# Optimization experiments

Hardware: AMD Instinct MI355X
Metric: run time of the kernel (lower is better)

Reference implementation:

```python
import jax, jax.numpy as jnp
import numpy as np

N_NODES = 50000
N_EDGES = 800000


def gat_layer(x, src, dst, W, al, ar, b, activation):
    # x: [N, F_in], W: [F_in, H*D], al/ar: [H, D], b: [H*D]
    H, D = al.shape
    n = x.shape[0]
    h = (x @ W).reshape(n, H, D)                      # [N, H, D]
    el = jnp.sum(h * al, axis=-1)                     # [N, H]
    er = jnp.sum(h * ar, axis=-1)                     # [N, H]
    e = jax.nn.leaky_relu(el[src] + er[dst], 0.2)     # [E, H]
    # segment softmax over incoming edges of each dst node
    m = jax.ops.segment_max(e, dst, num_segments=n)   # [N, H]
    ex = jnp.exp(e - m[dst])                          # [E, H]
    s = jax.ops.segment_sum(ex, dst, num_segments=n)  # [N, H]
    a = ex / s[dst]                                   # [E, H]
    msg = h[src] * a[:, :, None]                      # [E, H, D]
    out = jax.ops.segment_sum(msg, dst, num_segments=n) + b.reshape(1, H, D)
    return activation(out) if activation is not None else out


def setup_inputs() -> dict:
    key = jax.random.key(0)
    ks = jax.random.split(key, 12)
    feat = jax.random.normal(ks[0], (N_NODES, 128), dtype=jnp.float32)
    src = jax.random.randint(ks[1], (N_EDGES,), 0, N_NODES)
    dst = jax.random.randint(ks[2], (N_EDGES,), 0, N_NODES)
    sc = 0.1
    return {
        "feat": feat, "src": src, "dst": dst,
        "W1": jax.random.normal(ks[3], (128, 256), jnp.float32) * sc,
        "al1": jax.random.normal(ks[4], (4, 64), jnp.float32) * sc,
        "ar1": jax.random.normal(ks[5], (4, 64), jnp.float32) * sc,
        "b1": jnp.zeros((256,), jnp.float32),
        "W2": jax.random.normal(ks[6], (256, 256), jnp.float32) * sc,
        "al2": jax.random.normal(ks[7], (4, 64), jnp.float32) * sc,
        "ar2": jax.random.normal(ks[8], (4, 64), jnp.float32) * sc,
        "b2": jnp.zeros((256,), jnp.float32),
        "W3": jax.random.normal(ks[9], (256, 8), jnp.float32) * sc,
        "al3": jax.random.normal(ks[10], (1, 8), jnp.float32) * sc,
        "ar3": jax.random.normal(ks[11], (1, 8), jnp.float32) * sc,
        "b3": jnp.zeros((8,), jnp.float32),
    }


def reference(feat, src, dst, W1, al1, ar1, b1, W2, al2, ar2, b2, W3, al3, ar3, b3):
    n = feat.shape[0]
    elu = jax.nn.elu
    h = gat_layer(feat, src, dst, W1, al1, ar1, b1, elu).reshape(n, -1)  # flatten heads
    h = gat_layer(h, src, dst, W2, al2, ar2, b2, elu).reshape(n, -1)
    h = gat_layer(h, src, dst, W3, al3, ar3, b3, None)                   # [N, 1, out]
    return h.mean(axis=1)                                               # head mean -> [N, out]
```

## Files before the change

### kernel.cpp

```cpp
#include <hip/hip_runtime.h>
#include <math.h>


typedef _Float16 half8 __attribute__((ext_vector_type(8)));
typedef _Float16 half4 __attribute__((ext_vector_type(4)));
typedef float    floatx4 __attribute__((ext_vector_type(4)));

#define SLOT_CAP 48

__device__ __forceinline__ float leaky02(float x) { return x > 0.f ? x : 0.2f * x; }

__global__ void build_prep(const int* __restrict__ src, const int* __restrict__ dst,
                           int* __restrict__ cnt, unsigned short* __restrict__ slots,
                           const float* __restrict__ W1, _Float16* __restrict__ W1T,
                           const float* __restrict__ W2, _Float16* __restrict__ W2T,
                           int E, int GE) {
    int b = blockIdx.x;
    if (b < GE) {
        int i = b * 256 + threadIdx.x;
        if (i < E) {
            int d = dst[i];
            int p = atomicAdd(&cnt[d], 1);
            if (p < SLOT_CAP) slots[d * SLOT_CAP + p] = (unsigned short)src[i];
        }
    } else {
        int i = (b - GE) * 256 + threadIdx.x;
        if (i < 128 * 256) {
            int m = i >> 7, k = i & 127;
            W1T[i] = (_Float16)W1[k * 256 + m];
        } else {
            int j = i - 128 * 256;
            if (j < 256 * 256) {
                int m = j >> 8, k = j & 255;
                W2T[j] = (_Float16)W2[k * 256 + m];
            }
        }
    }
}

#define GBM 128
#define GBK 32

template <bool AF32>
__global__ __launch_bounds__(256)
void gemm_mfma(const void* __restrict__ Ap, const _Float16* __restrict__ BT,
               _Float16* __restrict__ C, int N, int K) {
    __shared__ _Float16 As[GBM][GBK + 8];
    __shared__ _Float16 Bs[GBM][GBK + 8];
    int tid  = threadIdx.x;
    int wave = tid >> 6, lane = tid & 63;
    int quad = lane >> 4, l16 = lane & 15;
    int row0 = blockIdx.y * GBM;
    int col0 = blockIdx.x * GBM;

    floatx4 acc[8][2];
    #pragma unroll
    for (int i = 0; i < 8; ++i)
        #pragma unroll
        for (int j = 0; j < 2; ++j)
            #pragma unroll
            for (int e = 0; e < 4; ++e) acc[i][j][e] = 0.f;

    for (int k0 = 0; k0 < K; k0 += GBK) {
        if (AF32) {
            const float* Af = (const float*)Ap;
            #pragma unroll
            for (int it = 0; it < 4; ++it) {
                int s = it * 256 + tid;
                int r = s >> 3, off = (s & 7) * 4;
                float4 v = make_float4(0.f, 0.f, 0.f, 0.f);
                int gr = row0 + r;
                if (gr < N) v = *(const float4*)&Af[(size_t)gr * K + k0 + off];
                half4 hv;
                hv[0] = (_Float16)v.x; hv[1] = (_Float16)v.y;
                hv[2] = (_Float16)v.z; hv[3] = (_Float16)v.w;
                *(half4*)&As[r][off] = hv;
            }
        } else {
            const _Float16* Ah = (const _Float16*)Ap;
            #pragma unroll
            for (int it = 0; it < 2; ++it) {
                int s = it * 256 + tid;
                int r = s >> 2, off = (s & 3) * 8;
                half8 v;
                #pragma unroll
                for (int q = 0; q < 8; ++q) v[q] = (_Float16)0.f;
                int gr = row0 + r;
                if (gr < N) v = *(const half8*)&Ah[(size_t)gr * K + k0 + off];
                *(half8*)&As[r][off] = v;
            }
        }
        #pragma unroll
        for (int it = 0; it < 2; ++it) {
            int s = it * 256 + tid;
            int r = s >> 2, off = (s & 3) * 8;
            half8 w = *(const half8*)&BT[(size_t)(col0 + r) * K + k0 + off];
            *(half8*)&Bs[r][off] = w;
        }
        __syncthreads();
        half8 bfrag[2];
        #pragma unroll
        for (int ct = 0; ct < 2; ++ct)
            bfrag[ct] = *(const half8*)&Bs[wave * 32 + ct * 16 + l16][quad * 8];
        #pragma unroll
        for (int rt = 0; rt < 8; ++rt) {
            half8 afrag = *(const half8*)&As[rt * 16 + l16][quad * 8];
            acc[rt][0] = __builtin_amdgcn_mfma_f32_16x16x32_f16(afrag, bfrag[0], acc[rt][0], 0, 0, 0);
            acc[rt][1] = __builtin_amdgcn_mfma_f32_16x16x32_f16(afrag, bfrag[1], acc[rt][1], 0, 0, 0);
        }
        __syncthreads();
    }
    #pragma unroll
    for (int rt = 0; rt < 8; ++rt) {
        #pragma unroll
        for (int reg = 0; reg < 4; ++reg) {
            int gr = row0 + rt * 16 + quad * 4 + reg;
            if (gr < N) {
                #pragma unroll
                for (int ct = 0; ct < 2; ++ct) {
                    int gc = col0 + wave * 32 + ct * 16 + l16;
                    C[(size_t)gr * 256 + gc] = (_Float16)acc[rt][ct][reg];
                }
            }
        }
    }
}

__global__ __launch_bounds__(256)
void attn_lr(const _Float16* __restrict__ h16, const float* __restrict__ al,
             const float* __restrict__ ar, float* __restrict__ el,
             float* __restrict__ er, int NH) {
    int wid = (blockIdx.x * 256 + threadIdx.x) >> 6;
    int lane = threadIdx.x & 63;
    int r = lane >> 3, c = lane & 7;
    int row = wid * 8 + r;
    if (row >= NH) return;
    int hd = row & 3;
    half8 hv = *(const half8*)&h16[(size_t)row * 64 + c * 8];
    const float* alp = &al[hd * 64 + c * 8];
    const float* arp = &ar[hd * 64 + c * 8];
    float l = 0.f, rr = 0.f;
    #pragma unroll
    for (int q = 0; q < 8; ++q) {
        float v = (float)hv[q];
        l  += v * alp[q];
        rr += v * arp[q];
    }
    l  += __shfl_xor(l, 1);  l  += __shfl_xor(l, 2);  l  += __shfl_xor(l, 4);
    rr += __shfl_xor(rr, 1); rr += __shfl_xor(rr, 2); rr += __shfl_xor(rr, 4);
    if (c == 0) { el[row] = l; er[row] = rr; }
}

__global__ __launch_bounds__(256)
void gat_agg(const _Float16* __restrict__ h16, const float* __restrict__ el,
             const float* __restrict__ er, const int* __restrict__ cnt,
             const unsigned short* __restrict__ slots, const float* __restrict__ bias,
             _Float16* __restrict__ out, int N) {
    __shared__ int   sbuf[8][32];
    __shared__ float wbuf[8][32][4];
    int tid = threadIdx.x;
    int l32 = tid & 31;
    int g = tid >> 5;
    int node = blockIdx.x * 8 + g;
    if (node >= N) return;
    int deg = min(cnt[node], SLOT_CAP);
    int beg = node * SLOT_CAP, end = beg + deg;
    int hd = l32 >> 3;

    float4 ern4 = *(const float4*)&er[node * 4];
    float er0 = ern4.x, er1 = ern4.y, er2 = ern4.z, er3 = ern4.w;

    const _Float16* hb = h16 + l32 * 8;
    float acc[8] = {};

    if (deg <= 32) {
        bool act = l32 < deg;
        int sv = 0;
        float e0 = -INFINITY, e1 = -INFINITY, e2 = -INFINITY, e3 = -INFINITY;
        if (act) {
            sv = slots[beg + l32];
            float4 elv = *(const float4*)&el[sv * 4];
            e0 = leaky02(elv.x + er0);
            e1 = leaky02(elv.y + er1);
            e2 = leaky02(elv.z + er2);
            e3 = leaky02(elv.w + er3);
        }
        float m0 = e0, m1 = e1, m2 = e2, m3 = e3;
        #pragma unroll
        for (int msk = 1; msk < 32; msk <<= 1) {
            m0 = fmaxf(m0, __shfl_xor(m0, msk));
            m1 = fmaxf(m1, __shfl_xor(m1, msk));
            m2 = fmaxf(m2, __shfl_xor(m2, msk));
            m3 = fmaxf(m3, __shfl_xor(m3, msk));
        }
        float x0 = act ? __expf(e0 - m0) : 0.f;
        float x1 = act ? __expf(e1 - m1) : 0.f;
        float x2 = act ? __expf(e2 - m2) : 0.f;
        float x3 = act ? __expf(e3 - m3) : 0.f;
        float s0 = x0, s1 = x1, s2 = x2, s3 = x3;
        #pragma unroll
        for (int msk = 1; msk < 32; msk <<= 1) {
            s0 += __shfl_xor(s0, msk);
            s1 += __shfl_xor(s1, msk);
            s2 += __shfl_xor(s2, msk);
            s3 += __shfl_xor(s3, msk);
        }
        float i0 = s0 > 0.f ? 1.f / s0 : 0.f;
        float i1 = s1 > 0.f ? 1.f / s1 : 0.f;
        float i2 = s2 > 0.f ? 1.f / s2 : 0.f;
        float i3 = s3 > 0.f ? 1.f / s3 : 0.f;
        if (act) {
            sbuf[g][l32] = sv;
            wbuf[g][l32][0] = x0 * i0;
            wbuf[g][l32][1] = x1 * i1;
            wbuf[g][l32][2] = x2 * i2;
            wbuf[g][l32][3] = x3 * i3;
        }
        int t = 0;
        for (; t + 4 <= deg; t += 4) {
            int sa = sbuf[g][t],     sb = sbuf[g][t + 1];
            int sc = sbuf[g][t + 2], sd = sbuf[g][t + 3];
            float wa = wbuf[g][t][hd],     wb = wbuf[g][t + 1][hd];
            float wc = wbuf[g][t + 2][hd], wd = wbuf[g][t + 3][hd];
            half8 va = *(const half8*)&hb[(size_t)sa * 256];
            half8 vb = *(const half8*)&hb[(size_t)sb * 256];
            half8 vc = *(const half8*)&hb[(size_t)sc * 256];
            half8 vd = *(const half8*)&hb[(size_t)sd * 256];
            #pragma unroll
            for (int q = 0; q < 8; ++q)
                acc[q] += wa * (float)va[q] + wb * (float)vb[q]
                        + wc * (float)vc[q] + wd * (float)vd[q];
        }
        for (; t < deg; ++t) {
            int s = sbuf[g][t];
            float w = wbuf[g][t][hd];
            half8 v = *(const half8*)&hb[(size_t)s * 256];
            #pragma unroll
            for (int q = 0; q < 8; ++q) acc[q] += w * (float)v[q];
        }
    } else {
        float m0 = -INFINITY, m1 = -INFINITY, m2 = -INFINITY, m3 = -INFINITY;
        for (int j = beg + l32; j < end; j += 32) {
            int sv = slots[j];
            float4 elv = *(const float4*)&el[sv * 4];
            m0 = fmaxf(m0, leaky02(elv.x + er0));
            m1 = fmaxf(m1, leaky02(elv.y + er1));
            m2 = fmaxf(m2, leaky02(elv.z + er2));
            m3 = fmaxf(m3, leaky02(elv.w + er3));
        }
        #pragma unroll
        for (int msk = 1; msk < 32; msk <<= 1) {
            m0 = fmaxf(m0, __shfl_xor(m0, msk));
            m1 = fmaxf(m1, __shfl_xor(m1, msk));
            m2 = fmaxf(m2, __shfl_xor(m2, msk));
            m3 = fmaxf(m3, __shfl_xor(m3, msk));
        }
        float s0 = 0.f, s1 = 0.f, s2 = 0.f, s3 = 0.f;
        for (int j = beg + l32; j < end; j += 32) {
            int sv = slots[j];
            float4 elv = *(const float4*)&el[sv * 4];
            s0 += __expf(leaky02(elv.x + er0) - m0);
            s1 += __expf(leaky02(elv.y + er1) - m1);
            s2 += __expf(leaky02(elv.z + er2) - m2);
            s3 += __expf(leaky02(elv.w + er3) - m3);
        }
        #pragma unroll
        for (int msk = 1; msk < 32; msk <<= 1) {
            s0 += __shfl_xor(s0, msk);
            s1 += __shfl_xor(s1, msk);
            s2 += __shfl_xor(s2, msk);
            s3 += __shfl_xor(s3, msk);
        }
        float mh  = (hd & 2) ? ((hd & 1) ? m3 : m2) : ((hd & 1) ? m1 : m0);
        float sh_ = (hd & 2) ? ((hd & 1) ? s3 : s2) : ((hd & 1) ? s1 : s0);
        float erh = (hd & 2) ? ((hd & 1) ? er3 : er2) : ((hd & 1) ? er1 : er0);
        float ih  = sh_ > 0.f ? 1.f / sh_ : 0.f;
        int j = beg;
        for (; j + 4 <= end; j += 4) {
            int sa = slots[j], sb = slots[j + 1], sc = slots[j + 2], sd = slots[j + 3];
            float wa = __expf(leaky02(el[sa * 4 + hd] + erh) - mh) * ih;
            float wb = __expf(leaky02(el[sb * 4 + hd] + erh) - mh) * ih;
            float wc = __expf(leaky02(el[sc * 4 + hd] + erh) - mh) * ih;
            float wd = __expf(leaky02(el[sd * 4 + hd] + erh) - mh) * ih;
            half8 va = *(const half8*)&hb[(size_t)sa * 256];
            half8 vb = *(const half8*)&hb[(size_t)sb * 256];
            half8 vc = *(const half8*)&hb[(size_t)sc * 256];
            half8 vd = *(const half8*)&hb[(size_t)sd * 256];
            #pragma unroll
            for (int q = 0; q < 8; ++q)
                acc[q] += wa * (float)va[q] + wb * (float)vb[q]
                        + wc * (float)vc[q] + wd * (float)vd[q];
        }
        for (; j < end; ++j) {
            int sv = slots[j];
            float w = __expf(leaky02(el[sv * 4 + hd] + erh) - mh) * ih;
            half8 v = *(const half8*)&hb[(size_t)sv * 256];
            #pragma unroll
            for (int q = 0; q < 8; ++q) acc[q] += w * (float)v[q];
        }
    }

    half8 o;
    #pragma unroll
    for (int q = 0; q < 8; ++q) {
        float v = acc[q] + bias[l32 * 8 + q];
        v = v > 0.f ? v : (__expf(v) - 1.f);
        o[q] = (_Float16)v;
    }
    *(half8*)&out[(size_t)node * 256 + l32 * 8] = o;
}

__global__ __launch_bounds__(256)
void gemm3_attn(const _Float16* __restrict__ x, const float* __restrict__ W,
                const float* __restrict__ al, const float* __restrict__ ar,
                float* __restrict__ h3, float* __restrict__ el,
                float* __restrict__ er, int N) {
    int tid = threadIdx.x;
    int lane = tid & 63;
    int n = blockIdx.x * 4 + (tid >> 6);
    if (n >= N) return;
    float4 wr[8];
    const float4* Wp = (const float4*)&W[lane * 32];
    #pragma unroll
    for (int i = 0; i < 8; ++i) wr[i] = Wp[i];
    half4 xv = *(const half4*)&x[(size_t)n * 256 + lane * 4];
    float acc[8];
    #pragma unroll
    for (int d = 0; d < 8; ++d) acc[d] = 0.f;
    #pragma unroll
    for (int q = 0; q < 4; ++q) {
        float xq = (float)xv[q];
        float4 w0 = wr[q * 2], w1 = wr[q * 2 + 1];
        acc[0] += xq * w0.x; acc[1] += xq * w0.y;
        acc[2] += xq * w0.z; acc[3] += xq * w0.w;
        acc[4] += xq * w1.x; acc[5] += xq * w1.y;
        acc[6] += xq * w1.z; acc[7] += xq * w1.w;
    }
    #pragma unroll
    for (int d = 0; d < 8; ++d) {
        #pragma unroll
        for (int o = 32; o; o >>= 1) acc[d] += __shfl_down(acc[d], o);
    }
    if (lane == 0) {
        float l = 0.f, r = 0.f;
        #pragma unroll
        for (int d = 0; d < 8; ++d) {
            h3[n * 8 + d] = acc[d];
            l += acc[d] * al[d];
            r += acc[d] * ar[d];
        }
        el[n] = l;
        er[n] = r;
    }
}

__global__ __launch_bounds__(256)
void gat_agg3(const float* __restrict__ h3, const float* __restrict__ el,
              const float* __restrict__ er, const int* __restrict__ cnt,
              const unsigned short* __restrict__ slots, const float* __restrict__ bias,
              float* __restrict__ out, int N) {
    __shared__ int   sbuf3[4][64];
    __shared__ float wbuf3[4][64];
    int tid = threadIdx.x;
    int lane = tid & 63;
    int wv = tid >> 6;
    int n = blockIdx.x * 4 + wv;
    if (n >= N) return;
    int deg = min(cnt[n], SLOT_CAP);
    int beg = n * SLOT_CAP;
    float er_n = er[n];
    int g = lane >> 3, c = lane & 7;
    float acc = 0.f;
    bool act = lane < deg;
    int sv = 0;
    float e = -INFINITY;
    if (act) { sv = slots[beg + lane]; e = leaky02(el[sv] + er_n); }
    float mx = e;
    #pragma unroll
    for (int o = 1; o < 64; o <<= 1) mx = fmaxf(mx, __shfl_xor(mx, o));
    float ex = act ? __expf(e - mx) : 0.f;
    float sm = ex;
    #pragma unroll
    for (int o = 1; o < 64; o <<= 1) sm += __shfl_xor(sm, o);
    float inv = sm > 0.f ? 1.f / sm : 0.f;
    if (act) {
        sbuf3[wv][lane] = sv;
        wbuf3[wv][lane] = ex * inv;
    }
    for (int t = g; t < deg; t += 8) {
        int s = sbuf3[wv][t];
        float w = wbuf3[wv][t];
        acc += h3[s * 8 + c] * w;
    }
    acc += __shfl_xor(acc, 8);
    acc += __shfl_xor(acc, 16);
    acc += __shfl_xor(acc, 32);
    if (lane < 8) out[(size_t)n * 8 + lane] = acc + bias[lane];
}

static inline size_t align_up(size_t x, size_t a) { return (x + a - 1) & ~(a - 1); }

extern "C" void kernel_launch(void* const* d_in, const int* in_sizes, int n_in,
                              void* d_out, int out_size, void* d_ws, size_t ws_size,
                              hipStream_t stream) {
    const float* feat = (const float*)d_in[0];
    const int*   src  = (const int*)d_in[1];
    const int*   dst  = (const int*)d_in[2];
    const float* W1   = (const float*)d_in[3];
    const float* al1  = (const float*)d_in[4];
    const float* ar1  = (const float*)d_in[5];
    const float* b1   = (const float*)d_in[6];
    const float* W2   = (const float*)d_in[7];
    const float* al2  = (const float*)d_in[8];
    const float* ar2  = (const float*)d_in[9];
    const float* b2   = (const float*)d_in[10];
    const float* W3   = (const float*)d_in[11];
    const float* al3  = (const float*)d_in[12];
    const float* ar3  = (const float*)d_in[13];
    const float* b3   = (const float*)d_in[14];

    const int N = in_sizes[0] / 128;
    const int E = in_sizes[1];

    char* w = (char*)d_ws;
    _Float16* bufA16 = (_Float16*)w; w += align_up((size_t)N * 256 * 2, 256);
    _Float16* bufB16 = (_Float16*)w; w += align_up((size_t)N * 256 * 2, 256);
    _Float16* W1T    = (_Float16*)w; w += align_up((size_t)256 * 128 * 2, 256);
    _Float16* W2T    = (_Float16*)w; w += align_up((size_t)256 * 256 * 2, 256);
    float* el      = (float*)w; w += align_up((size_t)N * 4 * 4, 256);
    float* er      = (float*)w; w += align_up((size_t)N * 4 * 4, 256);
    int*   cnt     = (int*)w;   w += align_up((size_t)N * 4, 256);
    unsigned short* slots = (unsigned short*)w;
    w += align_up((size_t)N * SLOT_CAP * 2, 256);
    float* h3 = (float*)bufA16;
    (void)ws_size; (void)n_in; (void)out_size;

    const int GE = (E + 255) / 256;
    const int GT = (128 * 256 + 256 * 256 + 255) / 256;

    (void)hipMemsetAsync(cnt, 0, (size_t)N * 4, stream);
    build_prep<<<GE + GT, 256, 0, stream>>>(src, dst, cnt, slots,
                                            W1, W1T, W2, W2T, E, GE);

    dim3 ggrid(2, (N + GBM - 1) / GBM);
    const int GA = (N + 7) / 8;
    const int GL = (N * 4 + 31) / 32;

    gemm_mfma<true><<<ggrid, 256, 0, stream>>>(feat, W1T, bufA16, N, 128);
    attn_lr<<<GL, 256, 0, stream>>>(bufA16, al1, ar1, el, er, N * 4);
    gat_agg<<<GA, 256, 0, stream>>>(bufA16, el, er, cnt, slots, b1, bufB16, N);

    gemm_mfma<false><<<ggrid, 256, 0, stream>>>(bufB16, W2T, bufA16, N, 256);
    attn_lr<<<GL, 256, 0, stream>>>(bufA16, al2, ar2, el, er, N * 4);
    gat_agg<<<GA, 256, 0, stream>>>(bufA16, el, er, cnt, slots, b2, bufB16, N);

    gemm3_attn<<<(N + 3) / 4, 256, 0, stream>>>(bufB16, W3, al3, ar3, h3, el, er, N);
    gat_agg3<<<(N + 3) / 4, 256, 0, stream>>>(h3, el, er, cnt, slots, b3,
                                              (float*)d_out, N);
}
```

Measured before the change: 389.2 us.

## Fold attention projections into weights and compute el/er inside GEMM via MFMA

Precomputes W·al and W·ar as a small 16-column fp16 matrix during setup. The GEMM's column-block 0 then runs extra MFMAs to produce el/er directly. This removes the separate attn_lr kernel and its re-read of the N×256 fp16 activation for layers 1 and 2. In exchange, el/er are computed from fp16-rounded folded weights rather than from the rounded h, which changes numerics slightly, and half of the GEMM blocks carry extra work.

Result: no change. 391.0 us (+0.5%).

```diff
diff --git a/kernel.cpp b/kernel.cpp
--- a/kernel.cpp
+++ b/kernel.cpp
@@ -14,7 +14,10 @@
                            int* __restrict__ cnt, unsigned short* __restrict__ slots,
                            const float* __restrict__ W1, _Float16* __restrict__ W1T,
                            const float* __restrict__ W2, _Float16* __restrict__ W2T,
-                           int E, int GE) {
+                           const float* __restrict__ al1, const float* __restrict__ ar1,
+                           const float* __restrict__ al2, const float* __restrict__ ar2,
+                           _Float16* __restrict__ WlrT1, _Float16* __restrict__ WlrT2,
+                           int E, int GE, int GT) {
     int b = blockIdx.x;
     if (b < GE) {
         int i = b * 256 + threadIdx.x;
@@ -23,7 +26,7 @@
             int p = atomicAdd(&cnt[d], 1);
             if (p < SLOT_CAP) slots[d * SLOT_CAP + p] = (unsigned short)src[i];
         }
-    } else {
+    } else if (b < GE + GT) {
         int i = (b - GE) * 256 + threadIdx.x;
         if (i < 128 * 256) {
             int m = i >> 7, k = i & 127;
@@ -35,6 +38,34 @@
                 W2T[j] = (_Float16)W2[k * 256 + m];
             }
         }
+    } else {
+        int t = (b - GE - GT) * 256 + threadIdx.x;
+        if (t < 16 * 128) {
+            int k = t & 127, c = t >> 7;
+            float v = 0.f;
+            if (c < 8) {
+                int h = c & 3;
+                const float* a = (c < 4 ? al1 : ar1) + h * 64;
+                const float* wrow = W1 + k * 256 + h * 64;
+                #pragma unroll 8
+                for (int d = 0; d < 64; ++d) v += wrow[d] * a[d];
+            }
+            WlrT1[c * 128 + k] = (_Float16)v;
+        } else {
+            int e = t - 16 * 128;
+            if (e < 16 * 256) {
+                int k = e & 255, c = e >> 8;
+                float v = 0.f;
+                if (c < 8) {
+                    int h = c & 3;
+                    const float* a = (c < 4 ? al2 : ar2) + h * 64;
+                    const float* wrow = W2 + k * 256 + h * 64;
+                    #pragma unroll 8
+                    for (int d = 0; d < 64; ++d) v += wrow[d] * a[d];
+                }
+                WlrT2[c * 256 + k] = (_Float16)v;
+            }
+        }
     }
 }
 
@@ -44,7 +75,8 @@
 template <bool AF32>
 __global__ __launch_bounds__(256)
 void gemm_mfma(const void* __restrict__ Ap, const _Float16* __restrict__ BT,
-               _Float16* __restrict__ C, int N, int K) {
+               _Float16* __restrict__ C, const _Float16* __restrict__ WlrT,
+               float* __restrict__ el, float* __restrict__ er, int N, int K) {
     __shared__ _Float16 As[GBM][GBK + 8];
     __shared__ _Float16 Bs[GBM][GBK + 8];
     int tid  = threadIdx.x;
@@ -52,6 +84,7 @@
     int quad = lane >> 4, l16 = lane & 15;
     int row0 = blockIdx.y * GBM;
     int col0 = blockIdx.x * GBM;
+    const bool doLR = (blockIdx.x == 0);
 
     floatx4 acc[8][2];
     #pragma unroll
@@ -60,6 +93,11 @@
         for (int j = 0; j < 2; ++j)
             #pragma unroll
             for (int e = 0; e < 4; ++e) acc[i][j][e] = 0.f;
+    floatx4 accLR[2];
+    #pragma unroll
+    for (int i = 0; i < 2; ++i)
+        #pragma unroll
+        for (int e = 0; e < 4; ++e) accLR[i][e] = 0.f;
 
     for (int k0 = 0; k0 < K; k0 += GBK) {
         if (AF32) {
@@ -102,11 +140,16 @@
         #pragma unroll
         for (int ct = 0; ct < 2; ++ct)
             bfrag[ct] = *(const half8*)&Bs[wave * 32 + ct * 16 + l16][quad * 8];
+        half8 lrfrag;
+        if (doLR)
+            lrfrag = *(const half8*)&WlrT[(size_t)l16 * K + k0 + quad * 8];
         #pragma unroll
         for (int rt = 0; rt < 8; ++rt) {
             half8 afrag = *(const half8*)&As[rt * 16 + l16][quad * 8];
             acc[rt][0] = __builtin_amdgcn_mfma_f32_16x16x32_f16(afrag, bfrag[0], acc[rt][0], 0, 0, 0);
             acc[rt][1] = __builtin_amdgcn_mfma_f32_16x16x32_f16(afrag, bfrag[1], acc[rt][1], 0, 0, 0);
+            if (doLR && (rt >> 1) == wave)
+                accLR[rt & 1] = __builtin_amdgcn_mfma_f32_16x16x32_f16(afrag, lrfrag, accLR[rt & 1], 0, 0, 0);
         }
         __syncthreads();
     }
@@ -124,31 +167,21 @@
             }
         }
     }
-}
-
-__global__ __launch_bounds__(256)
-void attn_lr(const _Float16* __restrict__ h16, const float* __restrict__ al,
-             const float* __restrict__ ar, float* __restrict__ el,
-             float* __restrict__ er, int NH) {
-    int wid = (blockIdx.x * 256 + threadIdx.x) >> 6;
-    int lane = threadIdx.x & 63;
-    int r = lane >> 3, c = lane & 7;
-    int row = wid * 8 + r;
-    if (row >= NH) return;
-    int hd = row & 3;
-    half8 hv = *(const half8*)&h16[(size_t)row * 64 + c * 8];
-    const float* alp = &al[hd * 64 + c * 8];
-    const float* arp = &ar[hd * 64 + c * 8];
-    float l = 0.f, rr = 0.f;
-    #pragma unroll
-    for (int q = 0; q < 8; ++q) {
-        float v = (float)hv[q];
-        l  += v * alp[q];
-        rr += v * arp[q];
-    }
-    l  += __shfl_xor(l, 1);  l  += __shfl_xor(l, 2);  l  += __shfl_xor(l, 4);
-    rr += __shfl_xor(rr, 1); rr += __shfl_xor(rr, 2); rr += __shfl_xor(rr, 4);
-    if (c == 0) { el[row] = l; er[row] = rr; }
+    if (doLR) {
+        #pragma unroll
+        for (int i = 0; i < 2; ++i) {
+            int rt = wave * 2 + i;
+            #pragma unroll
+            for (int reg = 0; reg < 4; ++reg) {
+                int gr = row0 + rt * 16 + quad * 4 + reg;
+                if (gr < N) {
+                    float v = accLR[i][reg];
+                    if (l16 < 4)      el[gr * 4 + l16] = v;
+                    else if (l16 < 8) er[gr * 4 + (l16 - 4)] = v;
+                }
+            }
+        }
+    }
 }
 
 __global__ __launch_bounds__(256)
@@ -427,6 +460,8 @@
     _Float16* bufB16 = (_Float16*)w; w += align_up((size_t)N * 256 * 2, 256);
     _Float16* W1T    = (_Float16*)w; w += align_up((size_t)256 * 128 * 2, 256);
     _Float16* W2T    = (_Float16*)w; w += align_up((size_t)256 * 256 * 2, 256);
+    _Float16* WlrT1  = (_Float16*)w; w += align_up((size_t)16 * 128 * 2, 256);
+    _Float16* WlrT2  = (_Float16*)w; w += align_up((size_t)16 * 256 * 2, 256);
     float* el      = (float*)w; w += align_up((size_t)N * 4 * 4, 256);
     float* er      = (float*)w; w += align_up((size_t)N * 4 * 4, 256);
     int*   cnt     = (int*)w;   w += align_up((size_t)N * 4, 256);
@@ -437,21 +472,21 @@
 
     const int GE = (E + 255) / 256;
     const int GT = (128 * 256 + 256 * 256 + 255) / 256;
+    const int GG = (16 * 128 + 16 * 256 + 255) / 256;
 
     (void)hipMemsetAsync(cnt, 0, (size_t)N * 4, stream);
-    build_prep<<<GE + GT, 256, 0, stream>>>(src, dst, cnt, slots,
-                                            W1, W1T, W2, W2T, E, GE);
+    build_prep<<<GE + GT + GG, 256, 0, stream>>>(src, dst, cnt, slots,
+                                                 W1, W1T, W2, W2T,
+                                                 al1, ar1, al2, ar2,
+                                                 WlrT1, WlrT2, E, GE, GT);
 
     dim3 ggrid(2, (N + GBM - 1) / GBM);
     const int GA = (N + 7) / 8;
-    const int GL = (N * 4 + 31) / 32;
-
-    gemm_mfma<true><<<ggrid, 256, 0, stream>>>(feat, W1T, bufA16, N, 128);
-    attn_lr<<<GL, 256, 0, stream>>>(bufA16, al1, ar1, el, er, N * 4);
+
+    gemm_mfma<true><<<ggrid, 256, 0, stream>>>(feat, W1T, bufA16, WlrT1, el, er, N, 128);
     gat_agg<<<GA, 256, 0, stream>>>(bufA16, el, er, cnt, slots, b1, bufB16, N);
 
-    gemm_mfma<false><<<ggrid, 256, 0, stream>>>(bufB16, W2T, bufA16, N, 256);
-    attn_lr<<<GL, 256, 0, stream>>>(bufA16, al2, ar2, el, er, N * 4);
+    gemm_mfma<false><<<ggrid, 256, 0, stream>>>(bufB16, W2T, bufA16, WlrT2, el, er, N, 256);
     gat_agg<<<GA, 256, 0, stream>>>(bufA16, el, er, cnt, slots, b2, bufB16, N);
 
     gemm3_attn<<<(N + 3) / 4, 256, 0, stream>>>(bufB16, W3, al3, ar3, h3, el, er, N);
```
